# Kernel tuning notes

Hardware: AMD Instinct MI355X
Metric: run time of the kernel (lower is better)

The kernel has to match this reference:

```python
import jax, jax.numpy as jnp
import numpy as np

FG_WEIGHT = 13.0
BG_WEIGHT = 1.0
DOWNSAMPLE_FACTOR = 1

B, H, W = 16, 768, 2048
N_PER_IMG = 32


def setup_inputs() -> dict:
    key = jax.random.key(0)
    k_loss, kx1, ky1, kw, kh = jax.random.split(key, 5)
    loss = jax.random.normal(k_loss, (B, H, W), dtype=jnp.float32)
    n_total = B * N_PER_IMG
    # realistic in-frame boxes: x1 < x2 <= W, y1 < y2 <= H
    x1 = jax.random.uniform(kx1, (n_total,), minval=0.0, maxval=W - 256.0)
    y1 = jax.random.uniform(ky1, (n_total,), minval=0.0, maxval=H - 192.0)
    bw = jax.random.uniform(kw, (n_total,), minval=16.0, maxval=256.0)
    bh = jax.random.uniform(kh, (n_total,), minval=16.0, maxval=192.0)
    gt_boxes2d = jnp.stack([x1, y1, x1 + bw, y1 + bh], axis=1).astype(jnp.float32)
    return {"loss": loss, "gt_boxes2d": gt_boxes2d, "num_gt_per_img": N_PER_IMG}


def _compute_fg_mask(gt_boxes2d, num_gt_per_img, b, h, w):
    # boxes: (B*N, 4) -> (B, N, 4); floor mins, ceil maxes (matches torch .long() raster)
    boxes = gt_boxes2d / DOWNSAMPLE_FACTOR
    boxes = boxes.reshape(b, num_gt_per_img, 4)
    u1 = jnp.floor(boxes[..., 0]).astype(jnp.int32)  # (B, N)
    v1 = jnp.floor(boxes[..., 1]).astype(jnp.int32)
    u2 = jnp.ceil(boxes[..., 2]).astype(jnp.int32)
    v2 = jnp.ceil(boxes[..., 3]).astype(jnp.int32)
    rows = jnp.arange(h)  # (H,)
    cols = jnp.arange(w)  # (W,)
    # separable membership: (B, N, H) and (B, N, W)
    row_in = (rows[None, None, :] >= v1[..., None]) & (rows[None, None, :] < v2[..., None])
    col_in = (cols[None, None, :] >= u1[..., None]) & (cols[None, None, :] < u2[..., None])
    # union over boxes via a small matmul instead of a (B,N,H,W) intermediate
    overlap = jnp.einsum("bnh,bnw->bhw", row_in.astype(jnp.float32), col_in.astype(jnp.float32))
    return overlap > 0.0  # (B, H, W) bool


def reference(loss, gt_boxes2d, num_gt_per_img):
    b, h, w = loss.shape
    fg_mask = _compute_fg_mask(gt_boxes2d, num_gt_per_img, b, h, w)
    weights = jnp.where(fg_mask, FG_WEIGHT, BG_WEIGHT).astype(loss.dtype)
    # fg_mask.sum() + bg_mask.sum() == total pixel count
    num_pixels = jnp.asarray(b * h * w, dtype=loss.dtype)
    # fg_loss + bg_loss == sum(loss * weights) / num_pixels (masks partition the image)
    return jnp.sum(loss * weights) / num_pixels
```

## Files before the change

### kernel.cpp

```cpp
#include <hip/hip_runtime.h>

constexpr int Bv = 16, Hv = 768, Wv = 2048;
constexpr int ROWS_PER_BLOCK = 4;
constexpr int NROWS   = Bv * Hv;
constexpr int NBLOCKS = NROWS / ROWS_PER_BLOCK;
constexpr int MAXN    = 256;

__global__ __launch_bounds__(256) void balancer_main(
    const float* __restrict__ loss,
    const float* __restrict__ boxes,
    const int*   __restrict__ num_gt,
    double*      __restrict__ partials)
{
    const int tid  = threadIdx.x;
    const int row0 = blockIdx.x * ROWS_PER_BLOCK;
    const int b    = row0 / Hv;
    const int n    = num_gt[0];

    __shared__ float s_y1[MAXN], s_y2[MAXN];
    __shared__ int   s_x1[MAXN], s_x2[MAXN];
    __shared__ int   s_u1[MAXN], s_u2[MAXN];
    __shared__ int   s_cnt;

    for (int i = tid; i < n && i < MAXN; i += blockDim.x) {
        const float* bx = boxes + (size_t)(b * n + i) * 4;
        s_x1[i] = (int)floorf(bx[0]);
        s_y1[i] = bx[1];
        s_x2[i] = (int)ceilf(bx[2]);
        s_y2[i] = bx[3];
    }

    float sum = 0.0f;

    for (int r = 0; r < ROWS_PER_BLOCK; ++r) {
        const int row = row0 + r;
        const int h   = row - b * Hv;

        __syncthreads();
        if (tid == 0) s_cnt = 0;
        __syncthreads();

        for (int i = tid; i < n && i < MAXN; i += blockDim.x) {
            const int v1 = (int)floorf(s_y1[i]);
            const int v2 = (int)ceilf(s_y2[i]);
            if (h >= v1 && h < v2) {
                const int pos = atomicAdd(&s_cnt, 1);
                s_u1[pos] = s_x1[i];
                s_u2[pos] = s_x2[i];
            }
        }
        __syncthreads();
        const int m = s_cnt;

        const float4* rowp = (const float4*)(loss + (size_t)row * Wv);
        #pragma unroll
        for (int it = 0; it < Wv / (256 * 4); ++it) {
            const int    idx4 = it * 256 + tid;
            const float4 v    = rowp[idx4];
            const int    c0   = idx4 * 4;
            bool f0 = false, f1 = false, f2 = false, f3 = false;
            for (int i = 0; i < m; ++i) {
                const int u1 = s_u1[i], u2 = s_u2[i];
                f0 |= (c0     >= u1) & (c0     < u2);
                f1 |= (c0 + 1 >= u1) & (c0 + 1 < u2);
                f2 |= (c0 + 2 >= u1) & (c0 + 2 < u2);
                f3 |= (c0 + 3 >= u1) & (c0 + 3 < u2);
            }
            sum += v.x * (f0 ? 13.0f : 1.0f);
            sum += v.y * (f1 ? 13.0f : 1.0f);
            sum += v.z * (f2 ? 13.0f : 1.0f);
            sum += v.w * (f3 ? 13.0f : 1.0f);
        }
    }

    for (int off = 32; off > 0; off >>= 1)
        sum += __shfl_down(sum, off, 64);

    __shared__ float s_wsum[4];
    const int lane = tid & 63;
    const int wid  = tid >> 6;
    if (lane == 0) s_wsum[wid] = sum;
    __syncthreads();
    if (tid == 0) {
        double d = 0.0;
        #pragma unroll
        for (int wq = 0; wq < 4; ++wq) d += (double)s_wsum[wq];
        partials[blockIdx.x] = d;
    }
}

__global__ __launch_bounds__(256) void balancer_reduce(
    const double* __restrict__ partials, float* __restrict__ out)
{
    const int tid = threadIdx.x;
    double s = 0.0;
    for (int i = tid; i < NBLOCKS; i += 256) s += partials[i];
    for (int off = 32; off > 0; off >>= 1)
        s += __shfl_down(s, off, 64);
    __shared__ double sh[4];
    if ((tid & 63) == 0) sh[tid >> 6] = s;
    __syncthreads();
    if (tid == 0) {
        const double t = sh[0] + sh[1] + sh[2] + sh[3];
        out[0] = (float)(t / (double)((long long)Bv * Hv * Wv));
    }
}

extern "C" void kernel_launch(void* const* d_in, const int* in_sizes, int n_in,
                              void* d_out, int out_size, void* d_ws, size_t ws_size,
                              hipStream_t stream) {
    const float* loss   = (const float*)d_in[0];
    const float* boxes  = (const float*)d_in[1];
    const int*   num_gt = (const int*)d_in[2];
    double*      partials = (double*)d_ws;
    float*       out      = (float*)d_out;

    balancer_main<<<NBLOCKS, 256, 0, stream>>>(loss, boxes, num_gt, partials);
    balancer_reduce<<<1, 256, 0, stream>>>(partials, out);
}
```

Measured before the change: 153.5 us.

## Prefetch all row loads up front and build per-row box lists in one pass

All eight float4 loss loads for the block's four rows are now issued at kernel start, before any box processing, so memory latency overlaps with the box-list construction. The per-row box filtering is merged into a single pass that fills four shared lists with atomics, and the three barriers per row are replaced by two per block. Boxes are read as a single float4 and interval bounds are stored as int2. The trade-off is higher register pressure from holding 32 floats per thread, which could reduce occupancy.

```diff
diff --git a/kernel.cpp b/kernel.cpp
--- a/kernel.cpp
+++ b/kernel.cpp
@@ -15,56 +15,56 @@
     const int tid  = threadIdx.x;
     const int row0 = blockIdx.x * ROWS_PER_BLOCK;
     const int b    = row0 / Hv;
+    const int h0   = row0 - b * Hv;
     const int n    = num_gt[0];
 
-    __shared__ float s_y1[MAXN], s_y2[MAXN];
-    __shared__ int   s_x1[MAXN], s_x2[MAXN];
-    __shared__ int   s_u1[MAXN], s_u2[MAXN];
-    __shared__ int   s_cnt;
-
-    for (int i = tid; i < n && i < MAXN; i += blockDim.x) {
-        const float* bx = boxes + (size_t)(b * n + i) * 4;
-        s_x1[i] = (int)floorf(bx[0]);
-        s_y1[i] = bx[1];
-        s_x2[i] = (int)ceilf(bx[2]);
-        s_y2[i] = bx[3];
+    float4 vbuf[ROWS_PER_BLOCK][2];
+    const float4* base = (const float4*)(loss + (size_t)row0 * Wv);
+    #pragma unroll
+    for (int r = 0; r < ROWS_PER_BLOCK; ++r) {
+        #pragma unroll
+        for (int it = 0; it < 2; ++it)
+            vbuf[r][it] = base[r * (Wv / 4) + it * 256 + tid];
     }
 
-    float sum = 0.0f;
+    __shared__ int  s_cnt[ROWS_PER_BLOCK];
+    __shared__ int2 s_uv[ROWS_PER_BLOCK][MAXN];
 
-    for (int r = 0; r < ROWS_PER_BLOCK; ++r) {
-        const int row = row0 + r;
-        const int h   = row - b * Hv;
+    if (tid < ROWS_PER_BLOCK) s_cnt[tid] = 0;
+    __syncthreads();
 
-        __syncthreads();
-        if (tid == 0) s_cnt = 0;
-        __syncthreads();
-
-        for (int i = tid; i < n && i < MAXN; i += blockDim.x) {
-            const int v1 = (int)floorf(s_y1[i]);
-            const int v2 = (int)ceilf(s_y2[i]);
+    for (int i = tid; i < n && i < MAXN; i += 256) {
+        const float4 bx = ((const float4*)boxes)[b * n + i];
+        const int u1 = (int)floorf(bx.x);
+        const int v1 = (int)floorf(bx.y);
+        const int u2 = (int)ceilf(bx.z);
+        const int v2 = (int)ceilf(bx.w);
+        #pragma unroll
+        for (int r = 0; r < ROWS_PER_BLOCK; ++r) {
+            const int h = h0 + r;
             if (h >= v1 && h < v2) {
-                const int pos = atomicAdd(&s_cnt, 1);
-                s_u1[pos] = s_x1[i];
-                s_u2[pos] = s_x2[i];
+                const int pos = atomicAdd(&s_cnt[r], 1);
+                s_uv[r][pos] = make_int2(u1, u2);
             }
         }
-        __syncthreads();
-        const int m = s_cnt;
+    }
+    __syncthreads();
 
-        const float4* rowp = (const float4*)(loss + (size_t)row * Wv);
+    float sum = 0.0f;
+    #pragma unroll
+    for (int r = 0; r < ROWS_PER_BLOCK; ++r) {
+        const int m = s_cnt[r];
         #pragma unroll
-        for (int it = 0; it < Wv / (256 * 4); ++it) {
-            const int    idx4 = it * 256 + tid;
-            const float4 v    = rowp[idx4];
-            const int    c0   = idx4 * 4;
+        for (int it = 0; it < 2; ++it) {
+            const float4 v  = vbuf[r][it];
+            const int    c0 = (it * 256 + tid) * 4;
             bool f0 = false, f1 = false, f2 = false, f3 = false;
             for (int i = 0; i < m; ++i) {
-                const int u1 = s_u1[i], u2 = s_u2[i];
-                f0 |= (c0     >= u1) & (c0     < u2);
-                f1 |= (c0 + 1 >= u1) & (c0 + 1 < u2);
-                f2 |= (c0 + 2 >= u1) & (c0 + 2 < u2);
-                f3 |= (c0 + 3 >= u1) & (c0 + 3 < u2);
+                const int2 uv = s_uv[r][i];
+                f0 |= (c0     >= uv.x) & (c0     < uv.y);
+                f1 |= (c0 + 1 >= uv.x) & (c0 + 1 < uv.y);
+                f2 |= (c0 + 2 >= uv.x) & (c0 + 2 < uv.y);
+                f3 |= (c0 + 3 >= uv.x) & (c0 + 3 < uv.y);
             }
             sum += v.x * (f0 ? 13.0f : 1.0f);
             sum += v.y * (f1 ? 13.0f : 1.0f);
```

Result: slower. 159.9 us (+4.1%).
